# Performance work log

Measured on AMD Instinct MI355X. Metric: run time of the kernel, lower is better.

The kernel has to match this reference:

```python
import jax, jax.numpy as jnp
import numpy as np

N = 50000       # nodes
E = 1600000     # edges (avg degree 32)
DIN = 64
DOUT = 64
DE = 16
ATT_SLOPE = 0.2   # leaky_relu slope inside attention (GAT standard)
ACT_SLOPE = 0.01  # F.leaky_relu default between layers


def setup_inputs() -> dict:
    key = jax.random.key(0)
    ks = jax.random.split(key, 16)

    def lin(k, i, o):
        return jax.random.normal(k, (i, o), jnp.float32) / np.sqrt(i).astype(np.float32)

    def vec(k, d):
        return jax.random.normal(k, (d,), jnp.float32) / np.sqrt(d).astype(np.float32)

    return {
        "X": jax.random.normal(ks[0], (N, DIN), jnp.float32),
        "edge_index": jax.random.randint(ks[1], (2, E), 0, N),
        "edge_attr": jax.random.normal(ks[2], (E, DE), jnp.float32),
        # layer 1 params
        "W1": lin(ks[3], DIN, DOUT), "We1": lin(ks[4], DE, DOUT),
        "as1": vec(ks[5], DOUT), "ad1": vec(ks[6], DOUT), "ae1": vec(ks[7], DOUT),
        "b1": jnp.zeros((DOUT,), jnp.float32),
        # layer 2 params
        "W2": lin(ks[8], DOUT, DOUT), "We2": lin(ks[9], DE, DOUT),
        "as2": vec(ks[10], DOUT), "ad2": vec(ks[11], DOUT), "ae2": vec(ks[12], DOUT),
        "b2": jnp.zeros((DOUT,), jnp.float32),
    }


def _gat_conv(x, src, dst, edge_attr, W, We, a_s, a_d, a_e, b):
    """GATConv with edge features, softmax attention over dst neighborhoods, max aggregation."""
    n = x.shape[0]
    h = x @ W                      # [N, DOUT]
    e = edge_attr @ We             # [E, DOUT]
    # per-edge attention logits
    logits = jax.nn.leaky_relu((h @ a_s)[src] + (h @ a_d)[dst] + e @ a_e, ATT_SLOPE)  # [E]
    # numerically-stable segment softmax over destination node
    m = jax.ops.segment_max(logits, dst, num_segments=n)      # [N]
    p = jnp.exp(logits - m[dst])                               # [E]
    s = jax.ops.segment_sum(p, dst, num_segments=n)            # [N]
    att = p / jnp.maximum(s[dst], 1e-16)                       # [E]
    msg = (h[src] + e) * att[:, None]                          # [E, DOUT]
    out = jax.ops.segment_max(msg, dst, num_segments=n)        # [N, DOUT], -inf for empty
    out = jnp.where(jnp.isfinite(out), out, 0.0)
    return out + b


def reference(X, edge_index, edge_attr,
              W1, We1, as1, ad1, ae1, b1,
              W2, We2, as2, ad2, ae2, b2):
    src, dst = edge_index[0], edge_index[1]
    c1 = _gat_conv(X, src, dst, edge_attr, W1, We1, as1, ad1, ae1, b1)
    c1 = jax.nn.leaky_relu(c1, ACT_SLOPE)
    c2 = _gat_conv(c1, src, dst, edge_attr, W2, We2, as2, ad2, ae2, b2)
    c2 = jax.nn.leaky_relu(c2, ACT_SLOPE)
    return c2
```

## Files before the change

kernel.cpp:

```cpp
#include <hip/hip_runtime.h>
#include <cstdint>
#include <cstddef>

#define NN 50000
#define EE 1600000
#define D  64
#define DE 16

__device__ __forceinline__ float bf2f(unsigned short u) {
    return __uint_as_float(((unsigned)u) << 16);
}
__device__ __forceinline__ unsigned short f2bf(float f) {
    unsigned u = __float_as_uint(f);
    unsigned r = u + 0x7FFFu + ((u >> 16) & 1u);
    return (unsigned short)(r >> 16);
}

__global__ void k_wae(const float* We1, const float* ae1,
                      const float* We2, const float* ae2,
                      float* wae ) {
    int t = threadIdx.x;
    if (t < 32) {
        const float* We = (t < 16) ? We1 : We2;
        const float* ae = (t < 16) ? ae1 : ae2;
        int k = t & 15;
        float acc = 0.f;
        for (int c = 0; c < D; c++) acc += We[k * D + c] * ae[c];
        wae[t] = acc;
    }
}

__global__ __launch_bounds__(256) void k_hist(const int* dst, int* counts) {
    int e = blockIdx.x * 256 + threadIdx.x;
    if (e < EE) atomicAdd(&counts[dst[e]], 1);
}

__global__ __launch_bounds__(256) void k_scanA(const int* counts, int* bsum) {
    __shared__ int tmp[256];
    int t = threadIdx.x, i = blockIdx.x * 256 + t;
    tmp[t] = (i < NN) ? counts[i] : 0;
    __syncthreads();
    for (int off = 128; off; off >>= 1) {
        if (t < off) tmp[t] += tmp[t + off];
        __syncthreads();
    }
    if (t == 0) bsum[blockIdx.x] = tmp[0];
}

__global__ __launch_bounds__(256) void k_scanB(int* bsum, int nchunks) {
    __shared__ int tmp[256];
    int t = threadIdx.x;
    int v = (t < nchunks) ? bsum[t] : 0;
    tmp[t] = v; __syncthreads();
    for (int off = 1; off < 256; off <<= 1) {
        int x = (t >= off) ? tmp[t - off] : 0;
        __syncthreads();
        tmp[t] += x;
        __syncthreads();
    }
    if (t < nchunks) bsum[t] = tmp[t] - v;
}

__global__ __launch_bounds__(256) void k_scanC(const int* counts, const int* bsumex,
                                               int* offsets, int* cursor) {
    __shared__ int tmp[256];
    int t = threadIdx.x, i = blockIdx.x * 256 + t;
    int v = (i < NN) ? counts[i] : 0;
    tmp[t] = v; __syncthreads();
    for (int off = 1; off < 256; off <<= 1) {
        int x = (t >= off) ? tmp[t - off] : 0;
        __syncthreads();
        tmp[t] += x;
        __syncthreads();
    }
    int excl = tmp[t] - v + bsumex[blockIdx.x];
    if (i < NN) { offsets[i] = excl; cursor[i] = excl; }
}

__global__ __launch_bounds__(256) void k_scatter(const int* src, const int* dst,
                                                 const float* ea, const float* wae,
                                                 int* cursor,
                                                 int* rsrc, int* reid,
                                                 float* ree1, float* ree2) {
    int e = blockIdx.x * 256 + threadIdx.x;
    if (e >= EE) return;
    int d = dst[e];
    const float4* rp = (const float4*)(ea + (size_t)e * DE);
    float4 q0 = rp[0], q1 = rp[1], q2 = rp[2], q3 = rp[3];
    float ev[16] = {q0.x, q0.y, q0.z, q0.w, q1.x, q1.y, q1.z, q1.w,
                    q2.x, q2.y, q2.z, q2.w, q3.x, q3.y, q3.z, q3.w};
    float e1 = 0.f, e2 = 0.f;
    #pragma unroll
    for (int j = 0; j < 16; j++) {
        e1 += ev[j] * wae[j];
        e2 += ev[j] * wae[16 + j];
    }
    int pos = atomicAdd(&cursor[d], 1);
    rsrc[pos] = src[e];
    reid[pos] = e;
    ree1[pos] = e1;
    ree2[pos] = e2;
}

template<int IN_BF16>
__global__ __launch_bounds__(256) void k_gemm(const void* xin, const float* W,
                                              const float* a_s, const float* a_d,
                                              unsigned short* h, float* hs, float* hd) {
    __shared__ float Wf[64][64];
    __shared__ float xs[4][64];
    int t = threadIdx.x, lane = t & 63, wv = t >> 6;
    for (int i = t; i < 4096; i += 256) Wf[i >> 6][i & 63] = W[i];
    float asl = a_s[lane];
    float adl = a_d[lane];
    __syncthreads();
    for (int n = blockIdx.x * 4 + wv; n < NN; n += gridDim.x * 4) {
        size_t idx = (size_t)n * D + lane;
        float xv = IN_BF16 ? bf2f(((const unsigned short*)xin)[idx])
                           : ((const float*)xin)[idx];
        xs[wv][lane] = xv;
        float acc = 0.f;
        #pragma unroll
        for (int k = 0; k < 64; k++) acc += xs[wv][k] * Wf[k][lane];
        h[idx] = f2bf(acc);
        float ps = acc * asl, pd = acc * adl;
        #pragma unroll
        for (int off = 32; off; off >>= 1) {
            ps += __shfl_xor(ps, off);
            pd += __shfl_xor(pd, off);
        }
        if (lane == 0) { hs[n] = ps; hd[n] = pd; }
    }
}

template<int OUT_F32>
__global__ __launch_bounds__(256) void k_gat(const int* rsrc, const int* reid, const float* ree,
                                             const int* offsets, const int* counts,
                                             const float* hs, const float* hd,
                                             const unsigned short* h, const float* ea,
                                             const float* We, const float* b,
                                             void* outv) {
    int t = threadIdx.x, lane = t & 63, wv = t >> 6;
    int g = lane >> 4, cl = lane & 15;

    float4 WelR[16];
    #pragma unroll
    for (int k = 0; k < 16; k++) WelR[k] = *(const float4*)(We + k * 64 + 4 * cl);

    int d = blockIdx.x * 4 + wv;
    int start = offsets[d];
    int deg = counts[d];
    float hdv = hd[d];

    float m = -__builtin_inff();
    float s = 0.f;
    for (int i = lane; i < deg; i += 64) {
        int sidx = start + i;
        int sr = rsrc[sidx];
        float ee = ree[sidx];
        float lg = hs[sr] + hdv + ee;
        lg = (lg >= 0.f) ? lg : 0.2f * lg;
        float mn = fmaxf(m, lg);
        s = ((m == mn) ? s : s * __expf(m - mn)) + __expf(lg - mn);
        m = mn;
    }
    #pragma unroll
    for (int off = 32; off; off >>= 1) {
        float m2 = __shfl_xor(m, off);
        float s2 = __shfl_xor(s, off);
        float mn = fmaxf(m, m2);
        float sa = (m == mn) ? s : s * __expf(m - mn);
        float sb = (m2 == mn) ? s2 : s2 * __expf(m2 - mn);
        s = sa + sb;
        m = mn;
    }
    float invs = 1.0f / fmaxf(s, 1e-16f);

    float a0 = -__builtin_inff(), a1 = a0, a2 = a0, a3 = a0;
    for (int i = 0; i < deg; i += 4) {
        int j = i + g;
        bool valid = (j < deg);
        int sidx = start + (valid ? j : 0);
        int sr  = rsrc[sidx];
        int eid = reid[sidx];
        float ee = ree[sidx];
        float hsv = hs[sr];
        const float4* ep = (const float4*)(ea + (size_t)eid * DE);
        float4 q0 = ep[0], q1 = ep[1], q2 = ep[2], q3 = ep[3];
        ushort4 hv = *(const ushort4*)(h + (size_t)sr * D + 4 * cl);

        float lg = hsv + hdv + ee;
        lg = (lg >= 0.f) ? lg : 0.2f * lg;
        float att = __expf(lg - m) * invs;

        float ear[16] = {q0.x, q0.y, q0.z, q0.w, q1.x, q1.y, q1.z, q1.w,
                         q2.x, q2.y, q2.z, q2.w, q3.x, q3.y, q3.z, q3.w};
        float e0 = 0.f, e1 = 0.f, e2 = 0.f, e3 = 0.f;
        #pragma unroll
        for (int k = 0; k < 16; k++) {
            e0 += ear[k] * WelR[k].x;
            e1 += ear[k] * WelR[k].y;
            e2 += ear[k] * WelR[k].z;
            e3 += ear[k] * WelR[k].w;
        }
        float v0 = (bf2f(hv.x) + e0) * att;
        float v1 = (bf2f(hv.y) + e1) * att;
        float v2 = (bf2f(hv.z) + e2) * att;
        float v3 = (bf2f(hv.w) + e3) * att;
        if (!valid) { v0 = v1 = v2 = v3 = -__builtin_inff(); }
        a0 = fmaxf(a0, v0); a1 = fmaxf(a1, v1);
        a2 = fmaxf(a2, v2); a3 = fmaxf(a3, v3);
    }
    #pragma unroll
    for (int off = 16; off <= 32; off <<= 1) {
        a0 = fmaxf(a0, __shfl_xor(a0, off));
        a1 = fmaxf(a1, __shfl_xor(a1, off));
        a2 = fmaxf(a2, __shfl_xor(a2, off));
        a3 = fmaxf(a3, __shfl_xor(a3, off));
    }

    if (g == 0) {
        float4 bl = *(const float4*)(b + 4 * cl);
        float o0 = ((deg > 0) ? a0 : 0.f) + bl.x;
        float o1 = ((deg > 0) ? a1 : 0.f) + bl.y;
        float o2 = ((deg > 0) ? a2 : 0.f) + bl.z;
        float o3 = ((deg > 0) ? a3 : 0.f) + bl.w;
        o0 = (o0 >= 0.f) ? o0 : 0.01f * o0;
        o1 = (o1 >= 0.f) ? o1 : 0.01f * o1;
        o2 = (o2 >= 0.f) ? o2 : 0.01f * o2;
        o3 = (o3 >= 0.f) ? o3 : 0.01f * o3;
        size_t oidx = (size_t)d * D + 4 * cl;
        if (OUT_F32) {
            *(float4*)((float*)outv + oidx) = make_float4(o0, o1, o2, o3);
        } else {
            ushort4 ov = {f2bf(o0), f2bf(o1), f2bf(o2), f2bf(o3)};
            *(ushort4*)((unsigned short*)outv + oidx) = ov;
        }
    }
}

extern "C" void kernel_launch(void* const* d_in, const int* in_sizes, int n_in,
                              void* d_out, int out_size, void* d_ws, size_t ws_size,
                              hipStream_t stream) {
    const float* X   = (const float*)d_in[0];
    const int*   eix = (const int*)d_in[1];
    const float* ea  = (const float*)d_in[2];
    const float* W1  = (const float*)d_in[3];
    const float* We1 = (const float*)d_in[4];
    const float* as1 = (const float*)d_in[5];
    const float* ad1 = (const float*)d_in[6];
    const float* ae1 = (const float*)d_in[7];
    const float* b1  = (const float*)d_in[8];
    const float* W2  = (const float*)d_in[9];
    const float* We2 = (const float*)d_in[10];
    const float* as2 = (const float*)d_in[11];
    const float* ad2 = (const float*)d_in[12];
    const float* ae2 = (const float*)d_in[13];
    const float* b2  = (const float*)d_in[14];

    const int* src = eix;
    const int* dst = eix + EE;

    char* w = (char*)d_ws;
    int*   rsrc = (int*)w;               w += (size_t)EE * 4;
    int*   reid = (int*)w;               w += (size_t)EE * 4;
    float* ree1 = (float*)w;             w += (size_t)EE * 4;
    float* ree2 = (float*)w;             w += (size_t)EE * 4;
    unsigned short* hA = (unsigned short*)w; w += (size_t)NN * D * 2;
    unsigned short* hB = (unsigned short*)w; w += (size_t)NN * D * 2;
    float* hs = (float*)w;               w += (size_t)NN * 4;
    float* hd = (float*)w;               w += (size_t)NN * 4;
    int* counts = (int*)w;               w += (size_t)NN * 4;
    int* offsets = (int*)w;              w += (size_t)NN * 4;
    int* cursor = (int*)w;               w += (size_t)NN * 4;
    int* bsum = (int*)w;                 w += 256 * 4;
    float* wae = (float*)w;              w += 32 * 4;

    const int nchunks = (NN + 255) / 256;

    hipMemsetAsync(counts, 0, (size_t)NN * 4, stream);
    k_wae<<<1, 64, 0, stream>>>(We1, ae1, We2, ae2, wae);
    k_hist<<<EE / 256, 256, 0, stream>>>(dst, counts);
    k_scanA<<<nchunks, 256, 0, stream>>>(counts, bsum);
    k_scanB<<<1, 256, 0, stream>>>(bsum, nchunks);
    k_scanC<<<nchunks, 256, 0, stream>>>(counts, bsum, offsets, cursor);
    k_scatter<<<EE / 256, 256, 0, stream>>>(src, dst, ea, wae, cursor,
                                            rsrc, reid, ree1, ree2);

    k_gemm<0><<<1024, 256, 0, stream>>>(X, W1, as1, ad1, hA, hs, hd);
    k_gat<0><<<NN / 4, 256, 0, stream>>>(rsrc, reid, ree1, offsets, counts, hs, hd,
                                         hA, ea, We1, b1, hB);
    k_gemm<1><<<1024, 256, 0, stream>>>(hB, W2, as2, ad2, hB, hs, hd);
    k_gat<1><<<NN / 4, 256, 0, stream>>>(rsrc, reid, ree2, offsets, counts, hs, hd,
                                         hB, ea, We2, b2, (float*)d_out);
}
```

Measured before the change: 688.6 us.

## Pack CSR edge records into int4, prefetch gather loads, register-resident GEMM weights

Edge metadata (source, edge id, and the two per-layer edge attention terms) is stored as one int4 record instead of four separate arrays, so each gather costs one 16-byte load. The GAT aggregation loop now software-prefetches the next edge's record, edge attributes, h row and hs value to hide gather latency. Zero-degree nodes exit early. The node GEMM keeps a weight column in registers and reads input rows with vector loads instead of going through shared memory. The trade-off is higher register pressure and wider records that waste bandwidth in layer-specific loops.

Measured after the change: 744.2 us. 8.1% more time.

```diff
diff --git a/kernel.cpp b/kernel.cpp
--- a/kernel.cpp
+++ b/kernel.cpp
@@ -79,9 +79,7 @@
 
 __global__ __launch_bounds__(256) void k_scatter(const int* src, const int* dst,
                                                  const float* ea, const float* wae,
-                                                 int* cursor,
-                                                 int* rsrc, int* reid,
-                                                 float* ree1, float* ree2) {
+                                                 int* cursor, int4* recs) {
     int e = blockIdx.x * 256 + threadIdx.x;
     if (e >= EE) return;
     int d = dst[e];
@@ -96,32 +94,44 @@
         e2 += ev[j] * wae[16 + j];
     }
     int pos = atomicAdd(&cursor[d], 1);
-    rsrc[pos] = src[e];
-    reid[pos] = e;
-    ree1[pos] = e1;
-    ree2[pos] = e2;
+    recs[pos] = make_int4(src[e], e, __float_as_int(e1), __float_as_int(e2));
 }
 
 template<int IN_BF16>
 __global__ __launch_bounds__(256) void k_gemm(const void* xin, const float* W,
                                               const float* a_s, const float* a_d,
                                               unsigned short* h, float* hs, float* hd) {
-    __shared__ float Wf[64][64];
-    __shared__ float xs[4][64];
-    int t = threadIdx.x, lane = t & 63, wv = t >> 6;
-    for (int i = t; i < 4096; i += 256) Wf[i >> 6][i & 63] = W[i];
-    float asl = a_s[lane];
-    float adl = a_d[lane];
-    __syncthreads();
-    for (int n = blockIdx.x * 4 + wv; n < NN; n += gridDim.x * 4) {
-        size_t idx = (size_t)n * D + lane;
-        float xv = IN_BF16 ? bf2f(((const unsigned short*)xin)[idx])
-                           : ((const float*)xin)[idx];
-        xs[wv][lane] = xv;
+    int t = threadIdx.x, lane = t & 63;
+    int wid0 = blockIdx.x * 4 + (t >> 6);
+    float Wcol[64];
+    #pragma unroll
+    for (int k = 0; k < 64; k++) Wcol[k] = W[k * 64 + lane];
+    float asl = a_s[lane], adl = a_d[lane];
+    for (int n0 = wid0; n0 < NN; n0 += 4096) {
+        int n = __builtin_amdgcn_readfirstlane(n0);
         float acc = 0.f;
-        #pragma unroll
-        for (int k = 0; k < 64; k++) acc += xs[wv][k] * Wf[k][lane];
-        h[idx] = f2bf(acc);
+        if (IN_BF16) {
+            const uint4* xr = (const uint4*)((const unsigned short*)xin + (size_t)n * 64);
+            #pragma unroll
+            for (int q = 0; q < 8; q++) {
+                uint4 u = xr[q];
+                unsigned uu[4] = {u.x, u.y, u.z, u.w};
+                #pragma unroll
+                for (int j = 0; j < 4; j++) {
+                    acc += bf2f((unsigned short)(uu[j] & 0xFFFFu)) * Wcol[q * 8 + 2 * j];
+                    acc += bf2f((unsigned short)(uu[j] >> 16))     * Wcol[q * 8 + 2 * j + 1];
+                }
+            }
+        } else {
+            const float4* xr = (const float4*)((const float*)xin + (size_t)n * 64);
+            #pragma unroll
+            for (int q = 0; q < 16; q++) {
+                float4 u = xr[q];
+                acc += u.x * Wcol[4 * q]     + u.y * Wcol[4 * q + 1]
+                     + u.z * Wcol[4 * q + 2] + u.w * Wcol[4 * q + 3];
+            }
+        }
+        h[(size_t)n * 64 + lane] = f2bf(acc);
         float ps = acc * asl, pd = acc * adl;
         #pragma unroll
         for (int off = 32; off; off >>= 1) {
@@ -132,13 +142,11 @@
     }
 }
 
-template<int OUT_F32>
-__global__ __launch_bounds__(256) void k_gat(const int* rsrc, const int* reid, const float* ree,
-                                             const int* offsets, const int* counts,
+template<int L2>
+__global__ __launch_bounds__(256) void k_gat(const int4* recs, const int* offsets, const int* counts,
                                              const float* hs, const float* hd,
                                              const unsigned short* h, const float* ea,
-                                             const float* We, const float* b,
-                                             void* outv) {
+                                             const float* We, const float* b, void* outv) {
     int t = threadIdx.x, lane = t & 63, wv = t >> 6;
     int g = lane >> 4, cl = lane & 15;
 
@@ -149,15 +157,32 @@
     int d = blockIdx.x * 4 + wv;
     int start = offsets[d];
     int deg = counts[d];
+
+    if (deg == 0) {
+        if (g == 0) {
+            float4 bl = *(const float4*)(b + 4 * cl);
+            float o0 = (bl.x >= 0.f) ? bl.x : 0.01f * bl.x;
+            float o1 = (bl.y >= 0.f) ? bl.y : 0.01f * bl.y;
+            float o2 = (bl.z >= 0.f) ? bl.z : 0.01f * bl.z;
+            float o3 = (bl.w >= 0.f) ? bl.w : 0.01f * bl.w;
+            size_t oidx = (size_t)d * D + 4 * cl;
+            if (L2) *(float4*)((float*)outv + oidx) = make_float4(o0, o1, o2, o3);
+            else {
+                ushort4 ov = {f2bf(o0), f2bf(o1), f2bf(o2), f2bf(o3)};
+                *(ushort4*)((unsigned short*)outv + oidx) = ov;
+            }
+        }
+        return;
+    }
+
     float hdv = hd[d];
 
     float m = -__builtin_inff();
     float s = 0.f;
     for (int i = lane; i < deg; i += 64) {
-        int sidx = start + i;
-        int sr = rsrc[sidx];
-        float ee = ree[sidx];
-        float lg = hs[sr] + hdv + ee;
+        int4 r = recs[start + i];
+        float ee = __int_as_float(L2 ? r.w : r.z);
+        float lg = hs[r.x] + hdv + ee;
         lg = (lg >= 0.f) ? lg : 0.2f * lg;
         float mn = fmaxf(m, lg);
         s = ((m == mn) ? s : s * __expf(m - mn)) + __expf(lg - mn);
@@ -175,25 +200,30 @@
     }
     float invs = 1.0f / fmaxf(s, 1e-16f);
 
+    int iters = (deg + 3) >> 2;
+    int4 rec = recs[start + min(g, deg - 1)];
+    const float4* ep = (const float4*)(ea + (size_t)rec.y * DE);
+    float4 A0 = ep[0], A1 = ep[1], A2 = ep[2], A3 = ep[3];
+    ushort4 HV = *(const ushort4*)(h + (size_t)rec.x * D + 4 * cl);
+    float HS = hs[rec.x];
+
     float a0 = -__builtin_inff(), a1 = a0, a2 = a0, a3 = a0;
-    for (int i = 0; i < deg; i += 4) {
-        int j = i + g;
-        bool valid = (j < deg);
-        int sidx = start + (valid ? j : 0);
-        int sr  = rsrc[sidx];
-        int eid = reid[sidx];
-        float ee = ree[sidx];
-        float hsv = hs[sr];
-        const float4* ep = (const float4*)(ea + (size_t)eid * DE);
-        float4 q0 = ep[0], q1 = ep[1], q2 = ep[2], q3 = ep[3];
-        ushort4 hv = *(const ushort4*)(h + (size_t)sr * D + 4 * cl);
-
-        float lg = hsv + hdv + ee;
+    for (int i = 0; i < iters; i++) {
+        int jn = min((i + 1) * 4 + g, deg - 1);
+        int4 recn = recs[start + jn];
+        const float4* epn = (const float4*)(ea + (size_t)recn.y * DE);
+        float4 B0 = epn[0], B1 = epn[1], B2 = epn[2], B3 = epn[3];
+        ushort4 HVn = *(const ushort4*)(h + (size_t)recn.x * D + 4 * cl);
+        float HSn = hs[recn.x];
+
+        bool valid = (i * 4 + g) < deg;
+        float ee = __int_as_float(L2 ? rec.w : rec.z);
+        float lg = HS + hdv + ee;
         lg = (lg >= 0.f) ? lg : 0.2f * lg;
         float att = __expf(lg - m) * invs;
 
-        float ear[16] = {q0.x, q0.y, q0.z, q0.w, q1.x, q1.y, q1.z, q1.w,
-                         q2.x, q2.y, q2.z, q2.w, q3.x, q3.y, q3.z, q3.w};
+        float ear[16] = {A0.x, A0.y, A0.z, A0.w, A1.x, A1.y, A1.z, A1.w,
+                         A2.x, A2.y, A2.z, A2.w, A3.x, A3.y, A3.z, A3.w};
         float e0 = 0.f, e1 = 0.f, e2 = 0.f, e3 = 0.f;
         #pragma unroll
         for (int k = 0; k < 16; k++) {
@@ -202,13 +232,15 @@
             e2 += ear[k] * WelR[k].z;
             e3 += ear[k] * WelR[k].w;
         }
-        float v0 = (bf2f(hv.x) + e0) * att;
-        float v1 = (bf2f(hv.y) + e1) * att;
-        float v2 = (bf2f(hv.z) + e2) * att;
-        float v3 = (bf2f(hv.w) + e3) * att;
+        float v0 = (bf2f(HV.x) + e0) * att;
+        float v1 = (bf2f(HV.y) + e1) * att;
+        float v2 = (bf2f(HV.z) + e2) * att;
+        float v3 = (bf2f(HV.w) + e3) * att;
         if (!valid) { v0 = v1 = v2 = v3 = -__builtin_inff(); }
         a0 = fmaxf(a0, v0); a1 = fmaxf(a1, v1);
         a2 = fmaxf(a2, v2); a3 = fmaxf(a3, v3);
+
+        rec = recn; A0 = B0; A1 = B1; A2 = B2; A3 = B3; HV = HVn; HS = HSn;
     }
     #pragma unroll
     for (int off = 16; off <= 32; off <<= 1) {
@@ -220,16 +252,13 @@
 
     if (g == 0) {
         float4 bl = *(const float4*)(b + 4 * cl);
-        float o0 = ((deg > 0) ? a0 : 0.f) + bl.x;
-        float o1 = ((deg > 0) ? a1 : 0.f) + bl.y;
-        float o2 = ((deg > 0) ? a2 : 0.f) + bl.z;
-        float o3 = ((deg > 0) ? a3 : 0.f) + bl.w;
+        float o0 = a0 + bl.x, o1 = a1 + bl.y, o2 = a2 + bl.z, o3 = a3 + bl.w;
         o0 = (o0 >= 0.f) ? o0 : 0.01f * o0;
         o1 = (o1 >= 0.f) ? o1 : 0.01f * o1;
         o2 = (o2 >= 0.f) ? o2 : 0.01f * o2;
         o3 = (o3 >= 0.f) ? o3 : 0.01f * o3;
         size_t oidx = (size_t)d * D + 4 * cl;
-        if (OUT_F32) {
+        if (L2) {
             *(float4*)((float*)outv + oidx) = make_float4(o0, o1, o2, o3);
         } else {
             ushort4 ov = {f2bf(o0), f2bf(o1), f2bf(o2), f2bf(o3)};
@@ -261,10 +290,7 @@
     const int* dst = eix + EE;
 
     char* w = (char*)d_ws;
-    int*   rsrc = (int*)w;               w += (size_t)EE * 4;
-    int*   reid = (int*)w;               w += (size_t)EE * 4;
-    float* ree1 = (float*)w;             w += (size_t)EE * 4;
-    float* ree2 = (float*)w;             w += (size_t)EE * 4;
+    int4* recs = (int4*)w;               w += (size_t)EE * 16;
     unsigned short* hA = (unsigned short*)w; w += (size_t)NN * D * 2;
     unsigned short* hB = (unsigned short*)w; w += (size_t)NN * D * 2;
     float* hs = (float*)w;               w += (size_t)NN * 4;
@@ -283,13 +309,11 @@
     k_scanA<<<nchunks, 256, 0, stream>>>(counts, bsum);
     k_scanB<<<1, 256, 0, stream>>>(bsum, nchunks);
     k_scanC<<<nchunks, 256, 0, stream>>>(counts, bsum, offsets, cursor);
-    k_scatter<<<EE / 256, 256, 0, stream>>>(src, dst, ea, wae, cursor,
-                                            rsrc, reid, ree1, ree2);
+    k_scatter<<<EE / 256, 256, 0, stream>>>(src, dst, ea, wae, cursor, recs);
 
     k_gemm<0><<<1024, 256, 0, stream>>>(X, W1, as1, ad1, hA, hs, hd);
-    k_gat<0><<<NN / 4, 256, 0, stream>>>(rsrc, reid, ree1, offsets, counts, hs, hd,
-                                         hA, ea, We1, b1, hB);
+    k_gat<0><<<NN / 4, 256, 0, stream>>>(recs, offsets, counts, hs, hd, hA, ea, We1, b1, hB);
     k_gemm<1><<<1024, 256, 0, stream>>>(hB, W2, as2, ad2, hB, hs, hd);
-    k_gat<1><<<NN / 4, 256, 0, stream>>>(rsrc, reid, ree2, offsets, counts, hs, hd,
-                                         hB, ea, We2, b2, (float*)d_out);
-}
+    k_gat<1><<<NN / 4, 256, 0, stream>>>(recs, offsets, counts, hs, hd, hB, ea, We2, b2,
+                                         (float*)d_out);
+}
```
